# Kernel tuning notes

Hardware: AMD Instinct MI355X
Metric: run time of the kernel (lower is better)

## Reference

```python
import jax, jax.numpy as jnp
import numpy as np

SOFTCAP = 50.0
EPS = 1e-6
N_HEADS, D_HEAD = 16, 64


def _rms(x, w):
    return x * jax.lax.rsqrt(jnp.mean(x * x, axis=-1, keepdims=True) + EPS) * w


def _rope(x, cos, sin):
    # Faithful to source: apply_rope uses x.size(1) as the position axis, but is
    # called on (B, H, T, Dh) tensors, so positions are indexed by HEAD index.
    n = x.shape[1]
    x1, x2 = x[..., 0::2], x[..., 1::2]
    c = cos[:n][None, :, None, :]
    s = sin[:n][None, :, None, :]
    return jnp.stack([x1 * c - x2 * s, x1 * s + x2 * c], axis=-1).reshape(x.shape)


def setup_inputs() -> dict:
    key = jax.random.key(0)
    ks = jax.random.split(key, 12)
    L, D, H, Dh, Dff, V, B, T = 6, 1024, N_HEADS, D_HEAD, 4096, 32000, 1, 1024
    r = lambda k, shape: jax.random.normal(k, shape, dtype=jnp.float32) * 0.02
    return {
        'x': jax.random.randint(ks[0], (B, T), 0, V, dtype=jnp.int32),
        'embed': r(ks[1], (V, D)),
        'ln1': jnp.ones((L, D), jnp.float32),
        'Wq': r(ks[2], (L, H * Dh, D)),
        'Wk': r(ks[3], (L, H * Dh, D)),
        'Wv': r(ks[4], (L, H * Dh, D)),
        'Wo': r(ks[5], (L, D, H * Dh)),
        'qn': jnp.ones((L, Dh), jnp.float32),
        'kn': jnp.ones((L, Dh), jnp.float32),
        'ln2': jnp.ones((L, D), jnp.float32),
        'Wg': r(ks[6], (L, Dff, D)),
        'Wu': r(ks[7], (L, Dff, D)),
        'Wd': r(ks[8], (L, D, Dff)),
        'ln_out': jnp.ones((D,), jnp.float32),
    }


def reference(x, embed, ln1, Wq, Wk, Wv, Wo, qn, kn, ln2, Wg, Wu, Wd, ln_out):
    B, T = x.shape
    H, Dh = N_HEADS, D_HEAD
    scale = Dh ** -0.5
    # RoPE tables (theta=10000)
    freqs = 1.0 / (10000.0 ** (jnp.arange(0, Dh, 2, dtype=jnp.float32) / Dh))
    ang = jnp.arange(T, dtype=jnp.float32)[:, None] * freqs[None, :]
    cos, sin = jnp.cos(ang), jnp.sin(ang)
    mask = jnp.triu(jnp.ones((T, T), dtype=bool), k=1)  # True above diagonal

    h = embed[x]  # (B, T, D)

    def block(h, p):
        l1, wq, wk, wv, wo, qnw, knw, l2, wg, wu, wd = p
        hn = _rms(h, l1)
        q = (hn @ wq.T).reshape(B, T, H, Dh).transpose(0, 2, 1, 3)  # (B,H,T,Dh)
        k = (hn @ wk.T).reshape(B, T, H, Dh).transpose(0, 2, 1, 3)
        v = (hn @ wv.T).reshape(B, T, H, Dh).transpose(0, 2, 1, 3)
        q = _rope(_rms(q, qnw), cos, sin)
        k = _rope(_rms(k, knw), cos, sin)
        scores = jnp.einsum('bhtd,bhsd->bhts', q, k) * scale
        scores = SOFTCAP * jnp.tanh(scores / SOFTCAP)
        scores = jnp.where(mask[None, None], -jnp.inf, scores)
        attn = jax.nn.softmax(scores, axis=-1)
        o = jnp.einsum('bhts,bhsd->bhtd', attn, v)
        o = o.transpose(0, 2, 1, 3).reshape(B, T, H * Dh)
        h = h + o @ wo.T
        hn2 = _rms(h, l2)
        h = h + (jax.nn.silu(hn2 @ wg.T) * (hn2 @ wu.T)) @ wd.T
        return h, None

    h, _ = jax.lax.scan(block, h, (ln1, Wq, Wk, Wv, Wo, qn, kn, ln2, Wg, Wu, Wd))
    # tied embed/head
    logits = _rms(h, ln_out) @ embed.T  # (B, T, V)
    return logits
```

## Files before the change

kernel.cpp:

```cpp
#include <hip/hip_runtime.h>
#include <math.h>
#include <type_traits>

typedef __bf16 bf16_t;
typedef bf16_t bf16x4 __attribute__((ext_vector_type(4)));
typedef bf16_t bf16x8 __attribute__((ext_vector_type(8)));
typedef float  f32x4  __attribute__((ext_vector_type(4)));

#define RMS_EPS 1e-6f

enum { EP_STORE = 0, EP_RESID = 1, EP_SPLIT = 2, EP_SILU = 3, EP_QKV = 4 };

template<int V> using IC = std::integral_constant<int, V>;

static __device__ __forceinline__ f32x4 mfma16(bf16x8 a, bf16x8 b, f32x4 c) {
    return __builtin_amdgcn_mfma_f32_16x16x32_bf16(a, b, c, 0, 0, 0);
}

#define GLDS(gp, lp) __builtin_amdgcn_global_load_lds( \
    (const __attribute__((address_space(1))) void*)(gp), \
    (__attribute__((address_space(3))) void*)(lp), 16, 0, 0)

template<int N> static __device__ __forceinline__ void vmwait() {
    if constexpr (N == 0)      asm volatile("s_waitcnt vmcnt(0)" ::: "memory");
    else if constexpr (N == 2) asm volatile("s_waitcnt vmcnt(2)" ::: "memory");
    else if constexpr (N == 3) asm volatile("s_waitcnt vmcnt(3)" ::: "memory");
    else if constexpr (N == 4) asm volatile("s_waitcnt vmcnt(4)" ::: "memory");
    else if constexpr (N == 6) asm volatile("s_waitcnt vmcnt(6)" ::: "memory");
    else if constexpr (N == 8) asm volatile("s_waitcnt vmcnt(8)" ::: "memory");
    __builtin_amdgcn_sched_barrier(0);
}
static __device__ __forceinline__ void bar() { __builtin_amdgcn_s_barrier(); }
static __device__ __forceinline__ void lgkm0() {
    asm volatile("s_waitcnt lgkmcnt(0)" ::: "memory");
    __builtin_amdgcn_sched_barrier(0);
}

template<int BM, int BN, int WR, int WC, int PLANES, int EPIL, int MINW, int DEPTH>
__global__ __launch_bounds__(WR * WC * 64, MINW)
void gemm_bf16(const bf16_t* __restrict__ Ah, const bf16_t* __restrict__ Al,
               const bf16_t* __restrict__ Bh,
               float* __restrict__ Cf, bf16_t* __restrict__ Ch, bf16_t* __restrict__ Cl,
               int K, int lda, int ldb, int ldc, long long sC,
               const float* __restrict__ qnw, const float* __restrict__ knw)
{
    constexpr int ASZ = BM * 32, BSZ = BN * 32;
    constexpr int NW = WR * WC;
    constexpr int NLD = (BM / 16 * (PLANES >= 2 ? 2 : 1) + BN / 16) / NW;
    __shared__ __align__(16) bf16_t sAh[DEPTH][ASZ], sBh[DEPTH][BSZ];
    __shared__ __align__(16) bf16_t sAl[PLANES >= 2 ? DEPTH : 1][PLANES >= 2 ? ASZ : 8];

    const int gx = gridDim.x;
    int id = blockIdx.x + gx * blockIdx.y;
    if (gridDim.z == 1) {
        int nwg = gx * gridDim.y;
        int q = nwg >> 3, r = nwg & 7;
        int xcd = id & 7, ix = id >> 3;
        id = (xcd < r ? xcd * (q + 1) : r * (q + 1) + (xcd - r) * q) + ix;
    }
    const int bm = id % gx, bn = id / gx;
    const int row0 = bm * BM, col0 = bn * BN;

    const size_t kofs = (size_t)blockIdx.z * K;
    Ah += kofs;  Bh += kofs;
    if constexpr (PLANES >= 2) Al += kofs;

    const int tid = threadIdx.x, lane = tid & 63, wave = tid >> 6;
    const int lr = lane & 15, lg = lane >> 4;
    constexpr int WM = BM / WR, WN = BN / WC, MF = WM / 16, NF = WN / 16;
    const int wr = wave / WC, wc = wave % WC;

    f32x4 acc[MF][NF];
    #pragma unroll
    for (int m = 0; m < MF; ++m)
        #pragma unroll
        for (int n = 0; n < NF; ++n) acc[m][n] = (f32x4){0.f, 0.f, 0.f, 0.f};

    auto stage = [&](int k0, int p) {
        #pragma unroll
        for (int i = wave; i < BM / 16; i += NW) {
            int s = i * 64 + lane, rr = s >> 2, c = s & 3;
            size_t go = (size_t)(row0 + rr) * lda + k0 + ((c ^ ((rr >> 1) & 3)) << 3);
            GLDS(Ah + go, &sAh[p][i * 512]);
            if constexpr (PLANES >= 2) GLDS(Al + go, &sAl[p][i * 512]);
        }
        #pragma unroll
        for (int i = wave; i < BN / 16; i += NW) {
            int s = i * 64 + lane, rr = s >> 2, c = s & 3;
            size_t go = (size_t)(col0 + rr) * ldb + k0 + ((c ^ ((rr >> 1) & 3)) << 3);
            GLDS(Bh + go, &sBh[p][i * 512]);
        }
    };

    auto compute = [&](int p) {
        bf16x8 ahf[MF], alf[MF], bhf[NF];
        #pragma unroll
        for (int m = 0; m < MF; ++m) {
            int rr = wr * WM + m * 16 + lr;
            int by = rr * 64 + ((lg ^ ((rr >> 1) & 3)) << 4);
            ahf[m] = *(const bf16x8*)((const char*)&sAh[p][0] + by);
            if constexpr (PLANES >= 2)
                alf[m] = *(const bf16x8*)((const char*)&sAl[p][0] + by);
        }
        #pragma unroll
        for (int n = 0; n < NF; ++n) {
            int rr = wc * WN + n * 16 + lr;
            int by = rr * 64 + ((lg ^ ((rr >> 1) & 3)) << 4);
            bhf[n] = *(const bf16x8*)((const char*)&sBh[p][0] + by);
        }
        #pragma unroll
        for (int m = 0; m < MF; ++m)
            #pragma unroll
            for (int n = 0; n < NF; ++n) {
                acc[m][n] = mfma16(ahf[m], bhf[n], acc[m][n]);
                if constexpr (PLANES >= 2)
                    acc[m][n] = mfma16(alf[m], bhf[n], acc[m][n]);
            }
    };

    if constexpr (DEPTH == 3) {
        const int NC = K >> 5;
        stage(0, 0);
        stage(32, 1);
        for (int j = 0; j + 2 < NC; ++j) {
            stage(32 * (j + 2), (j + 2) % 3);
            vmwait<2 * NLD>(); bar();
            compute(j % 3);
            bar();
        }
        vmwait<NLD>(); bar();
        compute((K >> 5) >= 2 ? ((K >> 5) - 2) % 3 : 0);
        vmwait<0>(); bar();
        compute(((K >> 5) - 1) % 3);
    } else {
        stage(0, 0);
        int k0 = 32;
        for (; k0 + 32 < K; k0 += 64) {
            stage(k0, 1);
            vmwait<NLD>(); bar();
            compute(0);
            bar();
            stage(k0 + 32, 0);
            vmwait<NLD>(); bar();
            compute(1);
            bar();
        }
        stage(k0, 1);
        vmwait<NLD>(); bar();
        compute(0);
        bar();
        vmwait<0>(); bar();
        compute(1);
    }

    if constexpr (EPIL == EP_QKV) {
        const int colbase = col0 + wc * WN;
        const int typ = colbase >> 10;
        if (typ < 2) {
            const float* nw = (typ == 0) ? qnw : knw;
            const int hh = (colbase - typ * 1024) >> 6;
            constexpr float kLogF = -0.41524101186092029f;
            #pragma unroll
            for (int m = 0; m < MF; ++m)
                #pragma unroll
                for (int r = 0; r < 4; ++r) {
                    int grow = row0 + wr * WM + m * 16 + lg * 4 + r;
                    float ss = 0.f;
                    #pragma unroll
                    for (int n = 0; n < NF; ++n) {
                        float v = acc[m][n][r];
                        ss += v * v;
                    }
                    ss += __shfl_xor(ss, 1, 64);
                    ss += __shfl_xor(ss, 2, 64);
                    ss += __shfl_xor(ss, 4, 64);
                    ss += __shfl_xor(ss, 8, 64);
                    float inv = rsqrtf(ss * (1.0f / 64.0f) + RMS_EPS);
                    #pragma unroll
                    for (int n = 0; n < NF; ++n) {
                        int i = n * 16 + lr;
                        float x = acc[m][n][r] * inv * nw[i];
                        float p = __shfl_xor(x, 1, 64);
                        float f = exp2f((float)(i >> 1) * kLogF);
                        float ang = (float)hh * f;
                        float cs = cosf(ang), sn = sinf(ang);
                        float o = (lr & 1) ? (p * sn + x * cs) : (x * cs - p * sn);
                        Ch[(size_t)grow * ldc + colbase + i] = (bf16_t)o;
                    }
                }
        } else {
            bf16_t* vTh_ = Cl;
            bf16_t* vTl_ = (bf16_t*)Cf;
            const int vcb = colbase - 2048;
            #pragma unroll
            for (int m = 0; m < MF; ++m)
                #pragma unroll
                for (int n = 0; n < NF; ++n) {
                    int vc = vcb + n * 16 + lr;
                    int grow0 = row0 + wr * WM + m * 16 + lg * 4;
                    bf16x4 hv, lv;
                    #pragma unroll
                    for (int r = 0; r < 4; ++r) {
                        float v = acc[m][n][r];
                        bf16_t hb = (bf16_t)v;
                        hv[r] = hb;
                        lv[r] = (bf16_t)(v - (float)hb);
                    }
                    *(bf16x4*)&vTh_[(size_t)vc * 1024 + grow0] = hv;
                    *(bf16x4*)&vTl_[(size_t)vc * 1024 + grow0] = lv;
                }
        }
        return;
    }

    #pragma unroll
    for (int m = 0; m < MF; ++m)
        #pragma unroll
        for (int n = 0; n < NF; ++n)
            #pragma unroll
            for (int r = 0; r < 4; ++r) {
                int grow = row0 + wr * WM + m * 16 + lg * 4 + r;
                int gcol = col0 + wc * WN + n * 16 + lr;
                float v = acc[m][n][r];
                size_t off = (size_t)blockIdx.z * sC + (size_t)grow * ldc + gcol;
                if constexpr (EPIL == EP_STORE) {
                    Cf[off] = v;
                } else if constexpr (EPIL == EP_RESID) {
                    Cf[off] += v;
                } else if constexpr (EPIL == EP_SPLIT) {
                    bf16_t hb = (bf16_t)v;
                    Ch[off] = hb;
                    Cl[off] = (bf16_t)(v - (float)hb);
                }
            }
}

__global__ __launch_bounds__(512, 4)
void gemm_gu_pack(const bf16_t* __restrict__ Ah, const bf16_t* __restrict__ Bh,
                  bf16_t* __restrict__ Ch,
                  const float* wq, const float* wk, const float* wv,
                  const float* wo, const float* wg, const float* wu,
                  const float* wd, bf16_t* wAd, bf16_t* wGUd, bf16_t* wdd)
{
    constexpr int lda = 1024, ldb = 1024, ldc = 4096, K = 1024;
    const int tid = threadIdx.x;

    if (blockIdx.z == 1) {
        if (!wq) return;
        int base = ((int)blockIdx.y * 8 + (int)blockIdx.x) * 512 + tid;
        #pragma unroll 4
        for (int j = 0; j < 32; ++j) {
            int v = j * 131072 + base;
            f32x4 val;
            bf16_t* dst;
            size_t doff;
            if (v < (1 << 20)) {
                int b = v >> 8, col = v & 255;
                const float* src = b < 1024 ? wq : b < 2048 ? wk : b < 3072 ? wv : wo;
                val = ((const f32x4*)src)[(size_t)(b & 1023) * 256 + col];
                dst = wAd; doff = (size_t)b * 256 + col;
            } else if (v < 3 * (1 << 20)) {
                int u = v - (1 << 20);
                int bb = u >> 8, col = u & 255;
                int row = bb < 4096 ? 2 * bb : 2 * (bb - 4096) + 1;
                const float* src = bb < 4096 ? wg : wu;
                val = ((const f32x4*)src)[(size_t)(bb & 4095) * 256 + col];
                dst = wGUd; doff = (size_t)row * 256 + col;
            } else {
                int u = v - 3 * (1 << 20);
                val = ((const f32x4*)wd)[u];
                dst = wdd; doff = (size_t)u;
            }
            bf16x4 hv;
            #pragma unroll
            for (int q2 = 0; q2 < 4; ++q2) hv[q2] = (bf16_t)val[q2];
            ((bf16x4*)dst)[doff] = hv;
        }
        return;
    }

    __shared__ __align__(16) bf16_t sA[3][128 * 32], sB[3][256 * 32];

    int id = blockIdx.x + 8 * blockIdx.y;
    {
        int q = 256 >> 3;
        int xcd = id & 7, ix = id >> 3;
        id = xcd * q + ix;
    }
    const int bm = id % 8, bn = id / 8;
    const int row0 = bm * 128, col0 = bn * 256;

    const int lane = tid & 63, wave = tid >> 6;
    const int lr = lane & 15, lg = lane >> 4;
    const int wr = wave >> 2, wc = wave & 3;

    f32x4 acc[4][4];
    #pragma unroll
    for (int m = 0; m < 4; ++m)
        #pragma unroll
        for (int n = 0; n < 4; ++n) acc[m][n] = (f32x4){0.f, 0.f, 0.f, 0.f};

    auto stage = [&](int k0, int p) {
        {
            int i = wave;
            int s = i * 64 + lane, rr = s >> 2, c = s & 3;
            size_t go = (size_t)(row0 + rr) * lda + k0 + ((c ^ ((rr >> 1) & 3)) << 3);
            GLDS(Ah + go, &sA[p][i * 512]);
        }
        #pragma unroll
        for (int i = wave; i < 16; i += 8) {
            int s = i * 64 + lane, rr = s >> 2, c = s & 3;
            size_t go = (size_t)(col0 + rr) * ldb + k0 + ((c ^ ((rr >> 1) & 3)) << 3);
            GLDS(Bh + go, &sB[p][i * 512]);
        }
    };

    auto compute = [&](int p) {
        bf16x8 af[4], bf4[4];
        #pragma unroll
        for (int m = 0; m < 4; ++m) {
            int rr = wr * 64 + m * 16 + lr;
            int by = rr * 64 + ((lg ^ ((rr >> 1) & 3)) << 4);
            af[m] = *(const bf16x8*)((const char*)&sA[p][0] + by);
        }
        #pragma unroll
        for (int n = 0; n < 4; ++n) {
            int rr = wc * 64 + n * 16 + lr;
            int by = rr * 64 + ((lg ^ ((rr >> 1) & 3)) << 4);
            bf4[n] = *(const bf16x8*)((const char*)&sB[p][0] + by);
        }
        #pragma unroll
        for (int m = 0; m < 4; ++m)
            #pragma unroll
            for (int n = 0; n < 4; ++n)
                acc[m][n] = mfma16(af[m], bf4[n], acc[m][n]);
    };

    const int NC = K >> 5;
    stage(0, 0);
    stage(32, 1);
    for (int j = 0; j + 2 < NC; ++j) {
        stage(32 * (j + 2), (j + 2) % 3);
        vmwait<6>(); bar();
        compute(j % 3);
        bar();
    }
    vmwait<3>(); bar();
    compute((NC - 2) % 3);
    vmwait<0>(); bar();
    compute((NC - 1) % 3);

    #pragma unroll
    for (int m = 0; m < 4; ++m)
        #pragma unroll
        for (int n = 0; n < 4; ++n)
            #pragma unroll
            for (int r = 0; r < 4; ++r) {
                int grow = row0 + wr * 64 + m * 16 + lg * 4 + r;
                int gcol = col0 + wc * 64 + n * 16 + lr;
                float v = acc[m][n][r];
                float pv = __shfl_xor(v, 1, 64);
                if (!(lr & 1)) {
                    float s = (v / (1.0f + __expf(-v))) * pv;
                    Ch[(size_t)grow * ldc + (gcol >> 1)] = (bf16_t)s;
                }
            }
}

__global__ __launch_bounds__(512, 2)
void gemm_logits8(const bf16_t* __restrict__ Ah, const bf16_t* __restrict__ Bh,
                  float* __restrict__ Cf)
{
    constexpr int lda = 1024, ldb = 1024, ldc = 32000;
    constexpr int NT = 16;
    __shared__ __align__(16) bf16_t sA[2][2][256 * 32];
    __shared__ __align__(16) bf16_t sB[2][2][256 * 32];

    const int gx = gridDim.x;
    int id = blockIdx.x + gx * blockIdx.y;
    {
        int nwg = gx * gridDim.y;
        int q = nwg >> 3, r = nwg & 7;
        int xcd = id & 7, ix = id >> 3;
        id = (xcd < r ? xcd * (q + 1) : r * (q + 1) + (xcd - r) * q) + ix;
    }
    const int bm = id % gx, bn = id / gx;
    const int row0 = bm * 256, col0 = bn * 256;

    const int tid = threadIdx.x, lane = tid & 63, wave = tid >> 6;
    const int lr = lane & 15, lg = lane >> 4;
    const int wr = wave >> 2, wc = wave & 3;

    f32x4 acc[8][4];
    #pragma unroll
    for (int m = 0; m < 8; ++m)
        #pragma unroll
        for (int n = 0; n < 4; ++n) acc[m][n] = (f32x4){0.f, 0.f, 0.f, 0.f};

    auto stageA = [&](int chunk, int buf, int ks) {
        int k0 = chunk * 32;
        #pragma unroll
        for (int i = wave; i < 16; i += 8) {
            int s = i * 64 + lane, rr = s >> 2, c = s & 3;
            size_t go = (size_t)(row0 + rr) * lda + k0 + ((c ^ ((rr >> 1) & 3)) << 3);
            GLDS(Ah + go, &sA[buf][ks][i * 512]);
        }
    };
    auto stageB = [&](int chunk, int buf, int ks) {
        int k0 = chunk * 32;
        #pragma unroll
        for (int i = wave; i < 16; i += 8) {
            int s = i * 64 + lane, rr = s >> 2, c = s & 3;
            size_t go = (size_t)(col0 + rr) * ldb + k0 + ((c ^ ((rr >> 1) & 3)) << 3);
            GLDS(Bh + go, &sB[buf][ks][i * 512]);
        }
    };

    auto phase = [&](int t, auto ksc) {
        constexpr int ks = decltype(ksc)::value;
        const int buf = t & 1;
        bf16x8 af[8], bf4[4];
        #pragma unroll
        for (int m = 0; m < 8; ++m) {
            int rr = wr * 128 + m * 16 + lr;
            int by = rr * 64 + ((lg ^ ((rr >> 1) & 3)) << 4);
            af[m] = *(const bf16x8*)((const char*)&sA[buf][ks][0] + by);
        }
        #pragma unroll
        for (int n = 0; n < 4; ++n) {
            int rr = wc * 64 + n * 16 + lr;
            int by = rr * 64 + ((lg ^ ((rr >> 1) & 3)) << 4);
            bf4[n] = *(const bf16x8*)((const char*)&sB[buf][ks][0] + by);
        }
        if constexpr (ks == 0) {
            if (t + 1 < NT) {
                stageA(2 * (t + 1) + 1, (t + 1) & 1, 1);
                stageB(2 * (t + 1) + 1, (t + 1) & 1, 1);
                vmwait<8>();
            } else {
                vmwait<0>();
            }
        } else {
            if (t + 2 < NT) {
                stageA(2 * (t + 2), t & 1, 0);
                stageB(2 * (t + 2), t & 1, 0);
                vmwait<8>();
            } else if (t + 1 < NT) {
                vmwait<4>();
            } else {
                vmwait<0>();
            }
        }
        bar();
        lgkm0();
        __builtin_amdgcn_s_setprio(1);
        #pragma unroll
        for (int m = 0; m < 8; ++m)
            #pragma unroll
            for (int n = 0; n < 4; ++n)
                acc[m][n] = mfma16(af[m], bf4[n], acc[m][n]);
        __builtin_amdgcn_s_setprio(0);
        bar();
    };

    stageA(0, 0, 0); stageB(0, 0, 0);
    stageA(1, 0, 1); stageB(1, 0, 1);
    stageA(2, 1, 0); stageB(2, 1, 0);
    vmwait<8>(); bar();

    for (int t = 0; t < NT; ++t) {
        phase(t, IC<0>{});
        phase(t, IC<1>{});
    }

    #pragma unroll
    for (int m = 0; m < 8; ++m)
        #pragma unroll
        for (int n = 0; n < 4; ++n)
            #pragma unroll
            for (int r = 0; r < 4; ++r) {
                int grow = row0 + wr * 128 + m * 16 + lg * 4 + r;
                int gcol = col0 + wc * 64 + n * 16 + lr;
                Cf[(size_t)grow * ldc + gcol] = acc[m][n][r];
            }
}

static __device__ __forceinline__ void wsplit_body(
    int b2, int tid,
    const float* wq, const float* wk, const float* wv, const float* wo,
    const float* wg, const float* wu, const float* wd,
    bf16_t* wAh, bf16_t* wGUh, bf16_t* wdh)
{
    #pragma unroll
    for (int k = 0; k < 4; ++k) {
        int b = b2 * 4 + k;
        const float* src;
        bf16_t* dst;
        size_t so, doff;
        if (b < 4096) {
            src = b < 1024 ? wq : b < 2048 ? wk : b < 3072 ? wv : wo;
            so = (size_t)(b & 1023) * 256 + tid;
            doff = (size_t)b * 256 + tid;
            dst = wAh;
        } else if (b < 12288) {
            int bb = b - 4096;
            int row = bb < 4096 ? 2 * bb : 2 * (bb - 4096) + 1;
            src = bb < 4096 ? wg : wu;
            so = (size_t)(bb & 4095) * 256 + tid;
            doff = (size_t)row * 256 + tid;
            dst = wGUh;
        } else {
            src = wd;
            so = (size_t)(b - 12288) * 256 + tid;
            doff = so;
            dst = wdh;
        }
        f32x4 v = ((const f32x4*)src)[so];
        bf16x4 hv;
        #pragma unroll
        for (int j = 0; j < 4; ++j) hv[j] = (bf16_t)v[j];
        ((bf16x4*)dst)[doff] = hv;
    }
}

__global__ __launch_bounds__(256)
void reduce_rms(const float* __restrict__ p, float* __restrict__ h,
                const float* __restrict__ w, bf16_t* __restrict__ outh)
{
    int blk = blockIdx.x, tid = threadIdx.x;
    size_t i = (size_t)blk * 256 + tid;
    const size_t S = (1024 * 1024) / 4;
    f32x4 a = ((const f32x4*)p)[i];
    f32x4 b = ((const f32x4*)p)[i + S];
    f32x4 c = ((const f32x4*)p)[i + 2 * S];
    f32x4 d = ((const f32x4*)p)[i + 3 * S];
    f32x4 hv = ((const f32x4*)h)[i];
    #pragma unroll
    for (int j = 0; j < 4; ++j) hv[j] += (a[j] + b[j]) + (c[j] + d[j]);
    ((f32x4*)h)[i] = hv;

    float ss = hv[0]*hv[0] + hv[1]*hv[1] + hv[2]*hv[2] + hv[3]*hv[3];
    #pragma unroll
    for (int m = 1; m < 64; m <<= 1) ss += __shfl_xor(ss, m, 64);
    __shared__ float red[4];
    if ((tid & 63) == 0) red[tid >> 6] = ss;
    __syncthreads();
    float tot = red[0] + red[1] + red[2] + red[3];
    float inv = rsqrtf(tot * (1.0f / 1024.0f) + RMS_EPS);
    f32x4 wt4 = *(const f32x4*)(w + tid * 4);
    bf16x4 hv4;
    #pragma unroll
    for (int j = 0; j < 4; ++j) hv4[j] = (bf16_t)(hv[j] * inv * wt4[j]);
    ((bf16x4*)outh)[i] = hv4;
}

__global__ __launch_bounds__(256)
void gather_rms_wsplit(const int* __restrict__ ids, const float* __restrict__ embed,
                       const float* __restrict__ w, float* __restrict__ h,
                       bf16_t* __restrict__ outh,
                       const float* wq, const float* wk, const float* wv,
                       const float* wo, const float* wg, const float* wu,
                       const float* wd, bf16_t* wAh, bf16_t* wGUh, bf16_t* wdh,
                       bf16_t* __restrict__ eh)
{
    int blk = blockIdx.x, tid = threadIdx.x;
    if (blk >= 5120) {
        int b2 = blk - 5120;
        #pragma unroll
        for (int k = 0; k < 4; ++k) {
            size_t so = ((size_t)b2 * 4 + k) * 256 + tid;
            f32x4 v = ((const f32x4*)embed)[so];
            bf16x4 hv;
            #pragma unroll
            for (int j = 0; j < 4; ++j) hv[j] = (bf16_t)v[j];
            ((bf16x4*)eh)[so] = hv;
        }
        return;
    }
    if (blk >= 1024) {
        wsplit_body(blk - 1024, tid, wq, wk, wv, wo, wg, wu, wd, wAh, wGUh, wdh);
        return;
    }
    int row = ids[blk];
    f32x4 v = ((const f32x4*)(embed + (size_t)row * 1024))[tid];
    ((f32x4*)(h + (size_t)blk * 1024))[tid] = v;

    float ss = v[0]*v[0] + v[1]*v[1] + v[2]*v[2] + v[3]*v[3];
    #pragma unroll
    for (int m = 1; m < 64; m <<= 1) ss += __shfl_xor(ss, m, 64);
    __shared__ float red[4];
    if ((tid & 63) == 0) red[tid >> 6] = ss;
    __syncthreads();
    float tot = red[0] + red[1] + red[2] + red[3];
    float inv = rsqrtf(tot * (1.0f / 1024.0f) + RMS_EPS);
    f32x4 wt4 = *(const f32x4*)(w + tid * 4);
    bf16x4 hv;
    #pragma unroll
    for (int j = 0; j < 4; ++j) hv[j] = (bf16_t)(v[j] * inv * wt4[j]);
    ((bf16x4*)outh)[(size_t)blk * 256 + tid] = hv;
}

__global__ __launch_bounds__(128, 2)
void flash_attn(const bf16_t* __restrict__ qkvh,
                const bf16_t* __restrict__ vTh, const bf16_t* __restrict__ vTl,
                bf16_t* __restrict__ oh)
{
    __shared__ __align__(16) bf16_t sQ[32*64], sK[64*64], sVh[64*64], sVl[64*64];
    __shared__ __align__(16) bf16_t sPh[32*64], sPl[32*64];

    const int q0 = blockIdx.x * 32;
    const int hh = blockIdx.y;
    const int tid = threadIdx.x, lane = tid & 63, w = tid >> 6;
    const int lr = lane & 15, lg = lane >> 4;

    #pragma unroll
    for (int ii = 0; ii < 2; ++ii) {
        int r0 = w * 16 + ii * 8;
        int r  = r0 + (lane >> 3);
        int i  = lane & 7;
        GLDS(qkvh + (size_t)(q0 + r) * 3072 + hh * 64 + ((i ^ (r & 7)) << 3),
             sQ + r0 * 64);
    }
    __syncthreads();

    bf16x8 qa[2];
    #pragma unroll
    for (int ks = 0; ks < 2; ++ks) {
        int r = w * 16 + lr;
        qa[ks] = *(const bf16x8*)((const char*)sQ + r * 128 +
                                  ((((ks << 2) | lg) ^ (r & 7)) << 4));
    }

    f32x4 o_acc[4];
    #pragma unroll
    for (int n = 0; n < 4; ++n) o_acc[n] = (f32x4){0.f, 0.f, 0.f, 0.f};
    float m_run[4] = {-1e30f, -1e30f, -1e30f, -1e30f};
    float l_run[4] = {0.f, 0.f, 0.f, 0.f};

    const int ntiles = ((q0 + 31) >> 6) + 1;
    for (int t = 0; t < ntiles; ++t) {
        const int kv0 = t * 64;
        #pragma unroll
        for (int ii = 0; ii < 4; ++ii) {
            int r0 = w * 32 + ii * 8;
            int r  = r0 + (lane >> 3);
            int i  = lane & 7;
            GLDS(qkvh + (size_t)(kv0 + r) * 3072 + 1024 + hh * 64 + ((i ^ (r & 7)) << 3),
                 sK + r0 * 64);
            GLDS(vTh + (size_t)(hh * 64 + r) * 1024 + kv0 + ((i ^ (r & 7)) << 3),
                 sVh + r0 * 64);
            GLDS(vTl + (size_t)(hh * 64 + r) * 1024 + kv0 + ((i ^ (r & 7)) << 3),
                 sVl + r0 * 64);
        }
        __syncthreads();

        f32x4 s_acc[4];
        #pragma unroll
        for (int n = 0; n < 4; ++n) s_acc[n] = (f32x4){0.f, 0.f, 0.f, 0.f};
        #pragma unroll
        for (int ks = 0; ks < 2; ++ks)
            #pragma unroll
            for (int n = 0; n < 4; ++n) {
                int r = n * 16 + lr;
                bf16x8 kb = *(const bf16x8*)((const char*)sK + r * 128 +
                                             ((((ks << 2) | lg) ^ (r & 7)) << 4));
                s_acc[n] = mfma16(qa[ks], kb, s_acc[n]);
            }

        #pragma unroll
        for (int j = 0; j < 4; ++j) {
            int qr = q0 + w * 16 + lg * 4 + j;
            float p[4];
            float mx = -1e30f;
            #pragma unroll
            for (int n = 0; n < 4; ++n) {
                float sx = s_acc[n][j] * (0.125f * 0.02f);
                float v = 50.f * (1.f - 2.f / (1.f + __expf(2.f * sx)));
                int key = kv0 + n * 16 + lr;
                if (key > qr) v = -1e30f;
                p[n] = v;
                mx = fmaxf(mx, v);
            }
            #pragma unroll
            for (int m = 1; m < 16; m <<= 1) mx = fmaxf(mx, __shfl_xor(mx, m, 64));
            float mn = fmaxf(m_run[j], mx);
            float ef = __expf(m_run[j] - mn);
            m_run[j] = mn;
            float rs = 0.f;
            #pragma unroll
            for (int n = 0; n < 4; ++n) {
                float e = __expf(p[n] - mn);
                p[n] = e;
                rs += e;
            }
            #pragma unroll
            for (int m = 1; m < 16; m <<= 1) rs += __shfl_xor(rs, m, 64);
            l_run[j] = l_run[j] * ef + rs;
            #pragma unroll
            for (int n = 0; n < 4; ++n) o_acc[n][j] *= ef;
            int r = w * 16 + lg * 4 + j;
            #pragma unroll
            for (int n = 0; n < 4; ++n) {
                int c = n * 16 + lr;
                int byo = r * 128 + ((((c >> 3) ^ (r & 7)) << 4)) + ((c & 7) << 1);
                bf16_t hb = (bf16_t)p[n];
                *(bf16_t*)((char*)sPh + byo) = hb;
                *(bf16_t*)((char*)sPl + byo) = (bf16_t)(p[n] - (float)hb);
            }
        }

        #pragma unroll
        for (int ks = 0; ks < 2; ++ks) {
            int pr = w * 16 + lr;
            int pby = pr * 128 + ((((ks << 2) | lg) ^ (pr & 7)) << 4);
            bf16x8 pa  = *(const bf16x8*)((const char*)sPh + pby);
            bf16x8 pl_ = *(const bf16x8*)((const char*)sPl + pby);
            #pragma unroll
            for (int n = 0; n < 4; ++n) {
                int vr = n * 16 + lr;
                int vby = vr * 128 + ((((ks << 2) | lg) ^ (vr & 7)) << 4);
                bf16x8 vhf = *(const bf16x8*)((const char*)sVh + vby);
                bf16x8 vlf = *(const bf16x8*)((const char*)sVl + vby);
                o_acc[n] = mfma16(pa,  vhf, o_acc[n]);
                o_acc[n] = mfma16(pl_, vhf, o_acc[n]);
                o_acc[n] = mfma16(pa,  vlf, o_acc[n]);
            }
        }
        __syncthreads();
    }

    #pragma unroll
    for (int j = 0; j < 4; ++j) {
        float inv = 1.0f / l_run[j];
        int qr = q0 + w * 16 + lg * 4 + j;
        #pragma unroll
        for (int n = 0; n < 4; ++n) {
            size_t off = (size_t)qr * 1024 + hh * 64 + n * 16 + lr;
            oh[off] = (bf16_t)(o_acc[n][j] * inv);
        }
    }
}

__global__ __launch_bounds__(256)
void rmsnorm_split(const float* __restrict__ in, const float* __restrict__ w,
                   bf16_t* __restrict__ outh)
{
    int row = blockIdx.x, tid = threadIdx.x;
    f32x4 v = *(const f32x4*)(in + (size_t)row * 1024 + tid * 4);
    float ss = v[0]*v[0] + v[1]*v[1] + v[2]*v[2] + v[3]*v[3];
    #pragma unroll
    for (int m = 1; m < 64; m <<= 1) ss += __shfl_xor(ss, m, 64);
    __shared__ float red[4];
    if ((tid & 63) == 0) red[tid >> 6] = ss;
    __syncthreads();
    float tot = red[0] + red[1] + red[2] + red[3];
    float inv = rsqrtf(tot * (1.0f / 1024.0f) + RMS_EPS);
    f32x4 wt4 = *(const f32x4*)(w + tid * 4);
    bf16x4 hv;
    #pragma unroll
    for (int j = 0; j < 4; ++j) hv[j] = (bf16_t)(v[j] * inv * wt4[j]);
    ((bf16x4*)outh)[(size_t)row * 256 + tid] = hv;
}

extern "C" void kernel_launch(void* const* d_in, const int* in_sizes, int n_in,
                              void* d_out, int out_size, void* d_ws, size_t ws_size,
                              hipStream_t stream)
{
    (void)in_sizes; (void)n_in; (void)out_size; (void)ws_size;
    const int*   x_ids = (const int*)  d_in[0];
    const float* embed = (const float*)d_in[1];
    const float* ln1   = (const float*)d_in[2];
    const float* Wq    = (const float*)d_in[3];
    const float* Wk    = (const float*)d_in[4];
    const float* Wv    = (const float*)d_in[5];
    const float* Wo    = (const float*)d_in[6];
    const float* qn    = (const float*)d_in[7];
    const float* kn    = (const float*)d_in[8];
    const float* ln2   = (const float*)d_in[9];
    const float* Wg    = (const float*)d_in[10];
    const float* Wu    = (const float*)d_in[11];
    const float* Wd    = (const float*)d_in[12];
    const float* lnout = (const float*)d_in[13];
    float* out = (float*)d_out;

    char* ws = (char*)d_ws;
    const size_t MB = 1 << 20;
    float*  h    = (float*) (ws +   0 * MB);
    bf16_t* hnh  = (bf16_t*)(ws +   4 * MB);
    bf16_t* qkvh = (bf16_t*)(ws +   8 * MB);
    bf16_t* vTh  = (bf16_t*)(ws +  20 * MB);
    bf16_t* vTl  = (bf16_t*)(ws +  22 * MB);
    bf16_t* oh   = (bf16_t*)(ws +  24 * MB);
    bf16_t* wA[2]  = {(bf16_t*)(ws +  28 * MB), (bf16_t*)(ws +  84 * MB)};
    bf16_t* wGU[2] = {(bf16_t*)(ws +  36 * MB), (bf16_t*)(ws +  92 * MB)};
    bf16_t* wD[2]  = {(bf16_t*)(ws +  52 * MB), (bf16_t*)(ws + 108 * MB)};
    bf16_t* silh = (bf16_t*)(ws +  60 * MB);
    float*  wdp  = (float*) (ws +  68 * MB);
    bf16_t* eh   = (bf16_t*)(ws + 116 * MB);

    const long long M1 = 1024 * 1024;

    gather_rms_wsplit<<<13120, 256, 0, stream>>>(
        x_ids, embed, ln1, h, hnh,
        Wq, Wk, Wv, Wo, Wg, Wu, Wd, wA[0], wGU[0], wD[0], eh);

    for (int l = 0; l < 6; ++l) {
        const int s = l & 1, nx = s ^ 1;

        gemm_bf16<64,128,2,2,1,EP_QKV,4,3><<<dim3(16,24),256,0,stream>>>(
            hnh, nullptr, wA[s], (float*)vTl, qkvh, vTh, 1024, 1024, 1024, 3072, 0,
            qn + l * 64, kn + l * 64);

        flash_attn<<<dim3(32,16), 128, 0, stream>>>(qkvh, vTh, vTl, oh);

        gemm_bf16<64,64,2,2,1,EP_RESID,4,3><<<dim3(16,16),256,0,stream>>>(
            oh, nullptr, wA[s] + 3 * M1, h, nullptr, nullptr, 1024, 1024, 1024, 1024, 0,
            nullptr, nullptr);

        rmsnorm_split<<<1024, 256, 0, stream>>>(h, ln2 + l * 1024, hnh);

        gemm_gu_pack<<<dim3(8,32,2), 512, 0, stream>>>(
            hnh, wGU[s], silh,
            l < 5 ? Wq + (size_t)(l+1) * M1 : nullptr,
            l < 5 ? Wk + (size_t)(l+1) * M1 : nullptr,
            l < 5 ? Wv + (size_t)(l+1) * M1 : nullptr,
            l < 5 ? Wo + (size_t)(l+1) * M1 : nullptr,
            l < 5 ? Wg + (size_t)(l+1) * 4 * M1 : nullptr,
            l < 5 ? Wu + (size_t)(l+1) * 4 * M1 : nullptr,
            l < 5 ? Wd + (size_t)(l+1) * 4 * M1 : nullptr,
            wA[nx], wGU[nx], wD[nx]);

        gemm_bf16<128,128,2,2,1,EP_STORE,4,3><<<dim3(8,8,4),256,0,stream>>>(
            silh, nullptr, wD[s], wdp, nullptr, nullptr, 1024, 4096, 4096, 1024, M1,
            nullptr, nullptr);

        const float* wnext = (l < 5) ? (ln1 + (l + 1) * 1024) : lnout;
        reduce_rms<<<1024, 256, 0, stream>>>(wdp, h, wnext, hnh);
    }

    gemm_logits8<<<dim3(4,125), 512, 0, stream>>>(hnh, eh, out);
}
```

Measured before the change: 1.125 ms.

## Spread embedding bf16 conversion across per-layer gate/up GEMM launches

The fp32-to-bf16 conversion of the 32000x1024 tied embedding table moves out of the initial gather kernel. It is split into six slices, each handled by an extra z-slice of blocks in the per-layer gate/up GEMM launch, so the conversion runs alongside the compute-bound GEMM instead of forming a bandwidth-bound prologue. The added blocks compete with the GEMM for CUs and memory bandwidth, and the slice bookkeeping (11 iterations of 131072 vectors per launch) must cover all 8,192,000 float4 vectors.

```diff
diff --git a/kernel.cpp b/kernel.cpp
--- a/kernel.cpp
+++ b/kernel.cpp
@@ -240,10 +240,27 @@
                   bf16_t* __restrict__ Ch,
                   const float* wq, const float* wk, const float* wv,
                   const float* wo, const float* wg, const float* wu,
-                  const float* wd, bf16_t* wAd, bf16_t* wGUd, bf16_t* wdd)
+                  const float* wd, bf16_t* wAd, bf16_t* wGUd, bf16_t* wdd,
+                  const float* __restrict__ embed, bf16_t* __restrict__ eh,
+                  int es, int ee)
 {
     constexpr int lda = 1024, ldb = 1024, ldc = 4096, K = 1024;
     const int tid = threadIdx.x;
+
+    if (blockIdx.z == 2) {
+        int base = ((int)blockIdx.y * 8 + (int)blockIdx.x) * 512 + tid;
+        for (int j = 0; j < 11; ++j) {
+            int u = es + j * 131072 + base;
+            if (u < ee) {
+                f32x4 v = ((const f32x4*)embed)[u];
+                bf16x4 hv;
+                #pragma unroll
+                for (int q2 = 0; q2 < 4; ++q2) hv[q2] = (bf16_t)v[q2];
+                ((bf16x4*)eh)[u] = hv;
+            }
+        }
+        return;
+    }
 
     if (blockIdx.z == 1) {
         if (!wq) return;
@@ -560,23 +577,9 @@
                        bf16_t* __restrict__ outh,
                        const float* wq, const float* wk, const float* wv,
                        const float* wo, const float* wg, const float* wu,
-                       const float* wd, bf16_t* wAh, bf16_t* wGUh, bf16_t* wdh,
-                       bf16_t* __restrict__ eh)
+                       const float* wd, bf16_t* wAh, bf16_t* wGUh, bf16_t* wdh)
 {
     int blk = blockIdx.x, tid = threadIdx.x;
-    if (blk >= 5120) {
-        int b2 = blk - 5120;
-        #pragma unroll
-        for (int k = 0; k < 4; ++k) {
-            size_t so = ((size_t)b2 * 4 + k) * 256 + tid;
-            f32x4 v = ((const f32x4*)embed)[so];
-            bf16x4 hv;
-            #pragma unroll
-            for (int j = 0; j < 4; ++j) hv[j] = (bf16_t)v[j];
-            ((bf16x4*)eh)[so] = hv;
-        }
-        return;
-    }
     if (blk >= 1024) {
         wsplit_body(blk - 1024, tid, wq, wk, wv, wo, wg, wu, wd, wAh, wGUh, wdh);
         return;
@@ -799,10 +802,12 @@
     bf16_t* eh   = (bf16_t*)(ws + 116 * MB);
 
     const long long M1 = 1024 * 1024;
-
-    gather_rms_wsplit<<<13120, 256, 0, stream>>>(
+    const int ETOT = 8192000;
+    const int ESL  = 1365334;
+
+    gather_rms_wsplit<<<5120, 256, 0, stream>>>(
         x_ids, embed, ln1, h, hnh,
-        Wq, Wk, Wv, Wo, Wg, Wu, Wd, wA[0], wGU[0], wD[0], eh);
+        Wq, Wk, Wv, Wo, Wg, Wu, Wd, wA[0], wGU[0], wD[0]);
 
     for (int l = 0; l < 6; ++l) {
         const int s = l & 1, nx = s ^ 1;
@@ -819,7 +824,8 @@
 
         rmsnorm_split<<<1024, 256, 0, stream>>>(h, ln2 + l * 1024, hnh);
 
-        gemm_gu_pack<<<dim3(8,32,2), 512, 0, stream>>>(
+        int es = l * ESL, ee = (l + 1) * ESL < ETOT ? (l + 1) * ESL : ETOT;
+        gemm_gu_pack<<<dim3(8,32,3), 512, 0, stream>>>(
             hnh, wGU[s], silh,
             l < 5 ? Wq + (size_t)(l+1) * M1 : nullptr,
             l < 5 ? Wk + (size_t)(l+1) * M1 : nullptr,
@@ -828,7 +834,8 @@
             l < 5 ? Wg + (size_t)(l+1) * 4 * M1 : nullptr,
             l < 5 ? Wu + (size_t)(l+1) * 4 * M1 : nullptr,
             l < 5 ? Wd + (size_t)(l+1) * 4 * M1 : nullptr,
-            wA[nx], wGU[nx], wD[nx]);
+            wA[nx], wGU[nx], wD[nx],
+            embed, eh, es, ee);
 
         gemm_bf16<128,128,2,2,1,EP_STORE,4,3><<<dim3(8,8,4),256,0,stream>>>(
             silh, nullptr, wD[s], wdp, nullptr, nullptr, 1024, 4096, 4096, 1024, M1,
```

Result: faster. 1.095 ms (-2.7%).
